# Performance work log

Measured on AMD Instinct MI355X. Metric: run time of the kernel, lower is better.

Reference implementation:

```python
import jax, jax.numpy as jnp
import numpy as np

N = 50000      # nodes
E = 800000     # edges (before self loops)
DIN = 128      # input feature dim
H = 2          # attention heads
C = 64         # per-head hidden channels (hidden_dim)
HC = H * C     # 128, concat output width of each GATv2 layer
DOUT = 4       # NUM_LANES
NEG = 0.2      # GATv2 default negative_slope


def _w(key, fan_in, shape):
    return jax.random.normal(key, shape, dtype=jnp.float32) * (1.0 / np.sqrt(fan_in))


def setup_inputs() -> dict:
    key = jax.random.key(0)
    ks = jax.random.split(key, 32)
    inp = {
        "x": jax.random.normal(ks[0], (N, DIN), dtype=jnp.float32),
        "edge_index": jax.random.randint(ks[1], (2, E), 0, N, dtype=jnp.int64),
    }
    # layer 1: DIN -> H*C
    inp["W1l"] = _w(ks[2], DIN, (DIN, HC)); inp["b1l"] = jnp.zeros((HC,), jnp.float32)
    inp["W1r"] = _w(ks[3], DIN, (DIN, HC)); inp["b1r"] = jnp.zeros((HC,), jnp.float32)
    inp["att1"] = _w(ks[4], C, (H, C));     inp["bias1"] = jnp.zeros((HC,), jnp.float32)
    # layer 2: H*C -> H*C
    inp["W2l"] = _w(ks[5], HC, (HC, HC));   inp["b2l"] = jnp.zeros((HC,), jnp.float32)
    inp["W2r"] = _w(ks[6], HC, (HC, HC));   inp["b2r"] = jnp.zeros((HC,), jnp.float32)
    inp["att2"] = _w(ks[7], C, (H, C));     inp["bias2"] = jnp.zeros((HC,), jnp.float32)
    # layer 3: H*C -> H*C
    inp["W3l"] = _w(ks[8], HC, (HC, HC));   inp["b3l"] = jnp.zeros((HC,), jnp.float32)
    inp["W3r"] = _w(ks[9], HC, (HC, HC));   inp["b3r"] = jnp.zeros((HC,), jnp.float32)
    inp["att3"] = _w(ks[10], C, (H, C));    inp["bias3"] = jnp.zeros((HC,), jnp.float32)
    # output linear
    inp["Wout"] = _w(ks[11], HC, (HC, DOUT)); inp["bout"] = jnp.zeros((DOUT,), jnp.float32)
    return inp


def gat_layer(x, src, dst, Wl, bl, Wr, br, att, bias):
    # GATv2Conv, concat=True, add_self_loops already in src/dst.
    n = x.shape[0]
    h, c = att.shape
    xl = (x @ Wl + bl).reshape(n, h, c)   # source transform
    xr = (x @ Wr + br).reshape(n, h, c)   # target transform
    m = xl[src] + xr[dst]                               # [Etot, H, C]
    e = jnp.sum(jax.nn.leaky_relu(m, NEG) * att, -1)    # [Etot, H]
    emax = jax.ops.segment_max(e, dst, num_segments=n)  # segment softmax over in-edges
    p = jnp.exp(e - emax[dst])
    denom = jax.ops.segment_sum(p, dst, num_segments=n)
    alpha = p / denom[dst]                              # [Etot, H]
    out = jax.ops.segment_sum(alpha[:, :, None] * xl[src], dst, num_segments=n)
    return out.reshape(n, h * c) + bias


def reference(x, edge_index, W1l, b1l, W1r, b1r, att1, bias1,
              W2l, b2l, W2r, b2r, att2, bias2,
              W3l, b3l, W3r, b3r, att3, bias3, Wout, bout):
    n = x.shape[0]
    loop = jnp.arange(n, dtype=edge_index.dtype)
    src = jnp.concatenate([edge_index[0], loop])  # add self loops (PyG default)
    dst = jnp.concatenate([edge_index[1], loop])
    h = jax.nn.relu(gat_layer(x, src, dst, W1l, b1l, W1r, b1r, att1, bias1))
    h = jax.nn.relu(gat_layer(h, src, dst, W2l, b2l, W2r, b2r, att2, bias2))
    h = jax.nn.relu(gat_layer(h, src, dst, W3l, b3l, W3r, b3r, att3, bias3))
    return h @ Wout + bout
```

## Files before the change

kernel.cpp:

```cpp
#include <hip/hip_runtime.h>
#include <math.h>

#define DIN  128
#define HC   128
#define NEG  0.2f

typedef __attribute__((ext_vector_type(8))) short bf16x8;
typedef __attribute__((ext_vector_type(4))) float f32x4;
typedef __attribute__((ext_vector_type(8))) _Float16 half8;
typedef __attribute__((ext_vector_type(2))) _Float16 half2v;

__device__ __forceinline__ unsigned short f2bf_rne(float x) {
    unsigned u = __float_as_uint(x);
    unsigned r = u + 0x7FFFu + ((u >> 16) & 1u);
    return (unsigned short)(r >> 16);
}
__device__ __forceinline__ float bf2f(unsigned short h) {
    return __uint_as_float(((unsigned)h) << 16);
}

__device__ __forceinline__ int colOf(int p) {
    return ((p >> 5) * 2 + (p & 1)) * 16 + ((p & 31) >> 1);
}

template <int CTRL>
__device__ __forceinline__ float dpp_xadd(float x) {
    int r = __builtin_amdgcn_update_dpp(0, __float_as_int(x), CTRL, 0xF, 0xF, true);
    return x + __int_as_float(r);
}
__device__ __forceinline__ float rowsum8(float x) {
    x = dpp_xadd<0xB1>(x);
    x = dpp_xadd<0x4E>(x);
    x = dpp_xadd<0x141>(x);
    return x;
}
__device__ __forceinline__ float rowsum16(float x) {
    x = dpp_xadd<0xB1>(x);
    x = dpp_xadd<0x4E>(x);
    x = dpp_xadd<0x141>(x);
    x = dpp_xadd<0x140>(x);
    return x;
}

__global__ void hist_kernel(const int* __restrict__ ei, int E, int N,
                            int* __restrict__ counts) {
    int i = blockIdx.x * blockDim.x + threadIdx.x;
    int Etot = E + N;
    if (i >= Etot) return;
    int dst = (i < E) ? ei[E + i] : (i - E);
    if (dst < 0 || dst >= N) return;
    atomicAdd(&counts[dst], 1);
}

__global__ void scan_kernel(const int* __restrict__ counts,
                            int* __restrict__ rowptr,
                            int* __restrict__ cursor, int n) {
    __shared__ int wsum[16];
    int tid  = threadIdx.x;
    int lane = tid & 63, wid = tid >> 6;
    int running = 0;
    for (int base = 0; base < n; base += 4096) {
        int i = base + tid * 4;
        int4 v = make_int4(0, 0, 0, 0);
        if (i < n) v = *(const int4*)&counts[i];
        int ssum = v.x + v.y + v.z + v.w;
        int x = ssum;
        #pragma unroll
        for (int off = 1; off < 64; off <<= 1) {
            int y = __shfl_up(x, off, 64);
            if (lane >= off) x += y;
        }
        if (lane == 63) wsum[wid] = x;
        __syncthreads();
        if (tid < 16) {
            int w = wsum[tid];
            #pragma unroll
            for (int off = 1; off < 16; off <<= 1) {
                int y = __shfl_up(w, off, 64);
                if (tid >= off) w += y;
            }
            wsum[tid] = w;
        }
        __syncthreads();
        int excl = running + (wid ? wsum[wid - 1] : 0) + (x - ssum);
        if (i < n) {
            int4 r;
            r.x = excl;
            r.y = r.x + v.x;
            r.z = r.y + v.y;
            r.w = r.z + v.z;
            *(int4*)&rowptr[i] = r;
            *(int4*)&cursor[i] = r;
        }
        running += wsum[15];
        __syncthreads();
    }
    if (tid == 0) rowptr[n] = running;
}

__global__ void scatter_kernel(const int* __restrict__ ei, int E, int N,
                               int* __restrict__ cursor,
                               int* __restrict__ esrc) {
    int i = blockIdx.x * blockDim.x + threadIdx.x;
    int Etot = E + N;
    if (i >= Etot) return;
    int src = (i < E) ? ei[i]     : (i - E);
    int dst = (i < E) ? ei[E + i] : (i - E);
    if (dst < 0 || dst >= N || src < 0 || src >= N) return;
    int pos = atomicAdd(&cursor[dst], 1);
    esrc[pos] = src;
}

__global__ __launch_bounds__(256) void prep_w(
        const float* __restrict__ W1l, const float* __restrict__ W1r,
        const float* __restrict__ W2l, const float* __restrict__ W2r,
        const float* __restrict__ W3l, const float* __restrict__ W3r,
        unsigned short* __restrict__ hi, unsigned short* __restrict__ lo) {
    int m = blockIdx.y;
    const float* W = (m == 0) ? W1l : (m == 1) ? W1r : (m == 2) ? W2l
                   : (m == 3) ? W2r : (m == 4) ? W3l : W3r;
    int t = blockIdx.x * 256 + threadIdx.x;
    int kb = t >> 9, nf = (t >> 6) & 7, l = t & 63;
    int col = nf * 16 + (l & 15);
    int k0  = kb * 32 + (l >> 4) * 8;
    size_t ob = ((size_t)m * 2048 + t) * 8;
    #pragma unroll
    for (int j = 0; j < 8; ++j) {
        int k = k0 + j;
        int krow = (m >= 2) ? colOf(k) : k;
        float v = W[(size_t)krow * 128 + col];
        unsigned short h = f2bf_rne(v);
        hi[ob + j] = h;
        lo[ob + j] = f2bf_rne(v - bf2f(h));
    }
}

__global__ __launch_bounds__(256) void gemm_mfma_dual(
        const float* __restrict__ X,
        const unsigned short* __restrict__ Whi,
        const unsigned short* __restrict__ Wlo, int matbase,
        const float* __restrict__ bl, const float* __restrict__ br,
        _Float16* __restrict__ xlh, _Float16* __restrict__ xrh, int nrows) {
    const unsigned short* hpl = Whi + ((size_t)(matbase + 0) * 16384);
    const unsigned short* lpl = Wlo + ((size_t)(matbase + 0) * 16384);
    const unsigned short* hpr = Whi + ((size_t)(matbase + 1) * 16384);
    const unsigned short* lpr = Wlo + ((size_t)(matbase + 1) * 16384);

    int tid = threadIdx.x;
    int w   = tid >> 6;
    int l   = tid & 63;
    int m15 = l & 15, g = l >> 4;
    int rowbase = blockIdx.x * 64 + w * 16;

    f32x4 accl[8], accr[8];
    #pragma unroll
    for (int nf = 0; nf < 8; ++nf) {
        accl[nf] = (f32x4){0.f, 0.f, 0.f, 0.f};
        accr[nf] = (f32x4){0.f, 0.f, 0.f, 0.f};
    }

    #pragma unroll
    for (int kb = 0; kb < 4; ++kb) {
        int arow = rowbase + m15;
        float4 x0 = make_float4(0.f, 0.f, 0.f, 0.f), x1 = x0;
        if (arow < nrows) {
            const float* xp = &X[(size_t)arow * 128 + kb * 32 + g * 8];
            x0 = *(const float4*)xp;
            x1 = *(const float4*)(xp + 4);
        }
        float xv[8] = {x0.x, x0.y, x0.z, x0.w, x1.x, x1.y, x1.z, x1.w};
        bf16x8 ahi, alo;
        #pragma unroll
        for (int j = 0; j < 8; ++j) {
            unsigned short h = f2bf_rne(xv[j]);
            ahi[j] = (short)h;
            alo[j] = (short)f2bf_rne(xv[j] - bf2f(h));
        }
        #pragma unroll
        for (int nf = 0; nf < 8; ++nf) {
            size_t off = (((size_t)kb * 8 + nf) * 64 + l) * 8;
            bf16x8 bhl = *(const bf16x8*)&hpl[off];
            bf16x8 bll = *(const bf16x8*)&lpl[off];
            bf16x8 bhr = *(const bf16x8*)&hpr[off];
            bf16x8 blr = *(const bf16x8*)&lpr[off];
            accl[nf] = __builtin_amdgcn_mfma_f32_16x16x32_bf16(ahi, bhl, accl[nf], 0, 0, 0);
            accl[nf] = __builtin_amdgcn_mfma_f32_16x16x32_bf16(ahi, bll, accl[nf], 0, 0, 0);
            accl[nf] = __builtin_amdgcn_mfma_f32_16x16x32_bf16(alo, bhl, accl[nf], 0, 0, 0);
            accr[nf] = __builtin_amdgcn_mfma_f32_16x16x32_bf16(ahi, bhr, accr[nf], 0, 0, 0);
            accr[nf] = __builtin_amdgcn_mfma_f32_16x16x32_bf16(ahi, blr, accr[nf], 0, 0, 0);
            accr[nf] = __builtin_amdgcn_mfma_f32_16x16x32_bf16(alo, bhr, accr[nf], 0, 0, 0);
        }
    }

    float vbl[8], vbr[8];
    #pragma unroll
    for (int nf = 0; nf < 8; ++nf) {
        vbl[nf] = bl[nf * 16 + m15];
        vbr[nf] = br[nf * 16 + m15];
    }

    #pragma unroll
    for (int a = 0; a < 4; ++a) {
        #pragma unroll
        for (int r = 0; r < 4; ++r) {
            int row = rowbase + g * 4 + r;
            if (row >= nrows) continue;
            size_t off = (size_t)row * 128 + a * 32 + m15 * 2;
            half2v pl, pr;
            pl[0] = (_Float16)(accl[2 * a][r]     + vbl[2 * a]);
            pl[1] = (_Float16)(accl[2 * a + 1][r] + vbl[2 * a + 1]);
            pr[0] = (_Float16)(accr[2 * a][r]     + vbr[2 * a]);
            pr[1] = (_Float16)(accr[2 * a + 1][r] + vbr[2 * a + 1]);
            *(half2v*)&xlh[off] = pl;
            *(half2v*)&xrh[off] = pr;
        }
    }
}

__global__ __launch_bounds__(256) void gat_aggregate(
        const _Float16* __restrict__ xlh, const _Float16* __restrict__ xrh,
        const int* __restrict__ rowptr, const int* __restrict__ esrc,
        const float* __restrict__ att, const float* __restrict__ bias,
        float* __restrict__ hout, int n, int do_relu,
        const float* __restrict__ Wout, const float* __restrict__ bout,
        float* __restrict__ out4) {
    int node = (int)((blockIdx.x * blockDim.x + threadIdx.x) >> 6);
    int lane = threadIdx.x & 63;
    if (node >= n) return;
    int g    = lane >> 4;
    int gl   = lane & 15;
    int pos0 = gl * 8;

    half8 xr8 = *(const half8*)&xrh[(size_t)node * 128 + pos0];
    float xrf[8], atp[8], atn[8];
    #pragma unroll
    for (int i = 0; i < 8; ++i) {
        float a = att[colOf(pos0 + i)];
        atp[i] = a;
        atn[i] = NEG * a;
        xrf[i] = (float)xr8[i];
    }

    float s = 0.f;
    float acc[8];
    #pragma unroll
    for (int i = 0; i < 8; ++i) acc[i] = 0.f;

    int pbeg = rowptr[node], pend = rowptr[node + 1];
    int p = pbeg + g;
    bool v0 = p < pend;
    bool v1 = p + 4 < pend;
    half8 r0 = (half8)(_Float16)0.f, r1 = r0;
    if (v0) r0 = *(const half8*)&xlh[(size_t)esrc[p] * 128 + pos0];
    if (v1) r1 = *(const half8*)&xlh[(size_t)esrc[p + 4] * 128 + pos0];

    while (v0) {
        bool v2 = p + 8 < pend;
        half8 r2 = (half8)(_Float16)0.f;
        if (v2) r2 = *(const half8*)&xlh[(size_t)esrc[p + 8] * 128 + pos0];

        float av[8], t = 0.f;
        #pragma unroll
        for (int i = 0; i < 8; ++i) {
            av[i] = (float)r0[i];
            float v = av[i] + xrf[i];
            t += v * (v > 0.f ? atp[i] : atn[i]);
        }
        t = rowsum8(t);
        float pp = __expf(fminf(t, 80.f));
        s += pp;
        #pragma unroll
        for (int i = 0; i < 8; ++i) acc[i] += pp * av[i];

        r0 = r1; r1 = r2; v0 = v1; v1 = v2; p += 4;
    }

    #pragma unroll
    for (int off = 16; off <= 32; off <<= 1) {
        s += __shfl_xor(s, off, 64);
        #pragma unroll
        for (int i = 0; i < 8; ++i) acc[i] += __shfl_xor(acc[i], off, 64);
    }

    float inv = 1.f / s;

    if (out4) {
        float o[8];
        #pragma unroll
        for (int i = 0; i < 8; ++i) {
            o[i] = acc[i] * inv + bias[colOf(pos0 + i)];
            if (do_relu) o[i] = fmaxf(o[i], 0.f);
        }
        float p0 = 0.f, p1 = 0.f, p2 = 0.f, p3 = 0.f;
        #pragma unroll
        for (int i = 0; i < 8; ++i) {
            float4 wv = *(const float4*)&Wout[colOf(pos0 + i) * 4];
            p0 += o[i] * wv.x; p1 += o[i] * wv.y;
            p2 += o[i] * wv.z; p3 += o[i] * wv.w;
        }
        p0 = rowsum16(p0); p1 = rowsum16(p1);
        p2 = rowsum16(p2); p3 = rowsum16(p3);
        if (lane == 0) {
            float4 ov = make_float4(p0 + bout[0], p1 + bout[1],
                                    p2 + bout[2], p3 + bout[3]);
            *(float4*)&out4[(size_t)node * 4] = ov;
        }
        return;
    }

    if (g == 0) {
        float o[8];
        #pragma unroll
        for (int i = 0; i < 8; ++i) {
            o[i] = acc[i] * inv + bias[colOf(pos0 + i)];
            if (do_relu) o[i] = fmaxf(o[i], 0.f);
        }
        float4 o0 = make_float4(o[0], o[1], o[2], o[3]);
        float4 o1 = make_float4(o[4], o[5], o[6], o[7]);
        *(float4*)&hout[(size_t)node * 128 + pos0]     = o0;
        *(float4*)&hout[(size_t)node * 128 + pos0 + 4] = o1;
    }
}

extern "C" void kernel_launch(void* const* d_in, const int* in_sizes, int n_in,
                              void* d_out, int out_size, void* d_ws,
                              size_t ws_size, hipStream_t stream) {
    const float* x    = (const float*)d_in[0];
    const int*   ei   = (const int*)  d_in[1];
    const float* W1l  = (const float*)d_in[2];
    const float* b1l  = (const float*)d_in[3];
    const float* W1r  = (const float*)d_in[4];
    const float* b1r  = (const float*)d_in[5];
    const float* att1 = (const float*)d_in[6];
    const float* bias1= (const float*)d_in[7];
    const float* W2l  = (const float*)d_in[8];
    const float* b2l  = (const float*)d_in[9];
    const float* W2r  = (const float*)d_in[10];
    const float* b2r  = (const float*)d_in[11];
    const float* att2 = (const float*)d_in[12];
    const float* bias2= (const float*)d_in[13];
    const float* W3l  = (const float*)d_in[14];
    const float* b3l  = (const float*)d_in[15];
    const float* W3r  = (const float*)d_in[16];
    const float* b3r  = (const float*)d_in[17];
    const float* att3 = (const float*)d_in[18];
    const float* bias3= (const float*)d_in[19];
    const float* Wout = (const float*)d_in[20];
    const float* bout = (const float*)d_in[21];

    int N    = in_sizes[0] / DIN;
    int E    = in_sizes[1] / 2;
    int Etot = E + N;

    char* base = (char*)d_ws;
    float* h = (float*)base;              base += (size_t)N * HC * 4;
    _Float16* xlh = (_Float16*)base;      base += (size_t)N * HC * 2;
    _Float16* xrh = (_Float16*)base;      base += (size_t)N * HC * 2;
    unsigned short* whi = (unsigned short*)base;  base += 6 * 16384 * 2;
    unsigned short* wlo = (unsigned short*)base;  base += 6 * 16384 * 2;
    int* esrc   = (int*)base;             base += (size_t)Etot * 4;
    int* rowptr = (int*)base;             base += (size_t)(((N + 1) + 3) & ~3) * 4;
    int* cursor = (int*)base;             base += (size_t)N * 4;
    int* counts = (int*)base;

    hipMemsetAsync(counts, 0, (size_t)N * sizeof(int), stream);
    hist_kernel<<<(Etot + 255) / 256, 256, 0, stream>>>(ei, E, N, counts);
    scan_kernel<<<1, 1024, 0, stream>>>(counts, rowptr, cursor, N);
    scatter_kernel<<<(Etot + 255) / 256, 256, 0, stream>>>(ei, E, N, cursor, esrc);
    prep_w<<<dim3(8, 6), 256, 0, stream>>>(W1l, W1r, W2l, W2r, W3l, W3r, whi, wlo);

    int gemm_grid = (N + 63) / 64;
    int agg_grid  = (N + 3) / 4;

    gemm_mfma_dual<<<gemm_grid, 256, 0, stream>>>(x, whi, wlo, 0, b1l, b1r, xlh, xrh, N);
    gat_aggregate<<<agg_grid, 256, 0, stream>>>(xlh, xrh, rowptr, esrc, att1, bias1,
                                                h, N, 1, nullptr, nullptr, nullptr);
    gemm_mfma_dual<<<gemm_grid, 256, 0, stream>>>(h, whi, wlo, 2, b2l, b2r, xlh, xrh, N);
    gat_aggregate<<<agg_grid, 256, 0, stream>>>(xlh, xrh, rowptr, esrc, att2, bias2,
                                                h, N, 1, nullptr, nullptr, nullptr);
    gemm_mfma_dual<<<gemm_grid, 256, 0, stream>>>(h, whi, wlo, 4, b3l, b3r, xlh, xrh, N);
    gat_aggregate<<<agg_grid, 256, 0, stream>>>(xlh, xrh, rowptr, esrc, att3, bias3,
                                                nullptr, N, 1, Wout, bout,
                                                (float*)d_out);
}
```

Before: 361.5 us.

## Switch GEMMs to single-pass fp16 MFMA and store hidden activations in fp16

Replaces the three-pass bf16 hi/lo split GEMM with a single fp16 MFMA pass using fp16-converted weights. Hidden activations between layers are stored as fp16 instead of fp32, which halves the write traffic in the aggregate kernel and the read traffic in the next GEMM. The GEMM tiling changes so that each block covers 32 rows and each wave handles half of the output columns. The cost is lower GEMM precision (fp16 inputs, about 11 bits of mantissa), with a risk of overflow or accuracy drift.

```diff
diff --git a/kernel.cpp b/kernel.cpp
--- a/kernel.cpp
+++ b/kernel.cpp
@@ -5,19 +5,9 @@
 #define HC   128
 #define NEG  0.2f
 
-typedef __attribute__((ext_vector_type(8))) short bf16x8;
 typedef __attribute__((ext_vector_type(4))) float f32x4;
 typedef __attribute__((ext_vector_type(8))) _Float16 half8;
 typedef __attribute__((ext_vector_type(2))) _Float16 half2v;
-
-__device__ __forceinline__ unsigned short f2bf_rne(float x) {
-    unsigned u = __float_as_uint(x);
-    unsigned r = u + 0x7FFFu + ((u >> 16) & 1u);
-    return (unsigned short)(r >> 16);
-}
-__device__ __forceinline__ float bf2f(unsigned short h) {
-    return __uint_as_float(((unsigned)h) << 16);
-}
 
 __device__ __forceinline__ int colOf(int p) {
     return ((p >> 5) * 2 + (p & 1)) * 16 + ((p & 31) >> 1);
@@ -111,11 +101,11 @@
     esrc[pos] = src;
 }
 
-__global__ __launch_bounds__(256) void prep_w(
+__global__ __launch_bounds__(256) void prep_w16(
         const float* __restrict__ W1l, const float* __restrict__ W1r,
         const float* __restrict__ W2l, const float* __restrict__ W2r,
         const float* __restrict__ W3l, const float* __restrict__ W3r,
-        unsigned short* __restrict__ hi, unsigned short* __restrict__ lo) {
+        _Float16* __restrict__ w16) {
     int m = blockIdx.y;
     const float* W = (m == 0) ? W1l : (m == 1) ? W1r : (m == 2) ? W2l
                    : (m == 3) ? W2r : (m == 4) ? W3l : W3r;
@@ -128,100 +118,96 @@
     for (int j = 0; j < 8; ++j) {
         int k = k0 + j;
         int krow = (m >= 2) ? colOf(k) : k;
-        float v = W[(size_t)krow * 128 + col];
-        unsigned short h = f2bf_rne(v);
-        hi[ob + j] = h;
-        lo[ob + j] = f2bf_rne(v - bf2f(h));
-    }
-}
-
-__global__ __launch_bounds__(256) void gemm_mfma_dual(
-        const float* __restrict__ X,
-        const unsigned short* __restrict__ Whi,
-        const unsigned short* __restrict__ Wlo, int matbase,
-        const float* __restrict__ bl, const float* __restrict__ br,
+        w16[ob + j] = (_Float16)W[(size_t)krow * 128 + col];
+    }
+}
+
+#define GEMM_BODY(A_LOAD)                                                     \
+    const _Float16* hpl = W16 + ((size_t)(matbase + 0) * 16384);              \
+    const _Float16* hpr = W16 + ((size_t)(matbase + 1) * 16384);              \
+    int tid = threadIdx.x;                                                    \
+    int w   = tid >> 6;                                                       \
+    int l   = tid & 63;                                                       \
+    int m15 = l & 15, g = l >> 4;                                             \
+    int rowbase = blockIdx.x * 32 + (w >> 1) * 16;                            \
+    int nfb     = (w & 1) * 4;                                                \
+    f32x4 accl[4], accr[4];                                                   \
+    _Pragma("unroll")                                                         \
+    for (int i = 0; i < 4; ++i) {                                             \
+        accl[i] = (f32x4){0.f, 0.f, 0.f, 0.f};                                \
+        accr[i] = (f32x4){0.f, 0.f, 0.f, 0.f};                                \
+    }                                                                         \
+    _Pragma("unroll")                                                         \
+    for (int kb = 0; kb < 4; ++kb) {                                          \
+        int arow = rowbase + m15;                                             \
+        half8 a16 = (half8)(_Float16)0.f;                                     \
+        A_LOAD                                                                \
+        _Pragma("unroll")                                                     \
+        for (int nfi = 0; nfi < 4; ++nfi) {                                   \
+            int nf = nfb + nfi;                                               \
+            size_t off = (((size_t)kb * 8 + nf) * 64 + l) * 8;                \
+            half8 b_l = *(const half8*)&hpl[off];                             \
+            half8 b_r = *(const half8*)&hpr[off];                             \
+            accl[nfi] = __builtin_amdgcn_mfma_f32_16x16x32_f16(a16, b_l, accl[nfi], 0, 0, 0); \
+            accr[nfi] = __builtin_amdgcn_mfma_f32_16x16x32_f16(a16, b_r, accr[nfi], 0, 0, 0); \
+        }                                                                     \
+    }                                                                         \
+    float vbl[4], vbr[4];                                                     \
+    _Pragma("unroll")                                                         \
+    for (int nfi = 0; nfi < 4; ++nfi) {                                       \
+        vbl[nfi] = bl[(nfb + nfi) * 16 + m15];                                \
+        vbr[nfi] = br[(nfb + nfi) * 16 + m15];                                \
+    }                                                                         \
+    _Pragma("unroll")                                                         \
+    for (int a2 = 0; a2 < 2; ++a2) {                                          \
+        int a = (nfb >> 1) + a2;                                              \
+        _Pragma("unroll")                                                     \
+        for (int r = 0; r < 4; ++r) {                                         \
+            int row = rowbase + g * 4 + r;                                    \
+            if (row >= nrows) continue;                                       \
+            size_t off = (size_t)row * 128 + a * 32 + m15 * 2;                \
+            half2v pl, pr;                                                    \
+            pl[0] = (_Float16)(accl[2 * a2][r]     + vbl[2 * a2]);            \
+            pl[1] = (_Float16)(accl[2 * a2 + 1][r] + vbl[2 * a2 + 1]);        \
+            pr[0] = (_Float16)(accr[2 * a2][r]     + vbr[2 * a2]);            \
+            pr[1] = (_Float16)(accr[2 * a2 + 1][r] + vbr[2 * a2 + 1]);        \
+            *(half2v*)&xlh[off] = pl;                                         \
+            *(half2v*)&xrh[off] = pr;                                         \
+        }                                                                     \
+    }
+
+__global__ __launch_bounds__(256) void gemm_f16_from_f32(
+        const float* __restrict__ X, const _Float16* __restrict__ W16,
+        int matbase, const float* __restrict__ bl, const float* __restrict__ br,
         _Float16* __restrict__ xlh, _Float16* __restrict__ xrh, int nrows) {
-    const unsigned short* hpl = Whi + ((size_t)(matbase + 0) * 16384);
-    const unsigned short* lpl = Wlo + ((size_t)(matbase + 0) * 16384);
-    const unsigned short* hpr = Whi + ((size_t)(matbase + 1) * 16384);
-    const unsigned short* lpr = Wlo + ((size_t)(matbase + 1) * 16384);
-
-    int tid = threadIdx.x;
-    int w   = tid >> 6;
-    int l   = tid & 63;
-    int m15 = l & 15, g = l >> 4;
-    int rowbase = blockIdx.x * 64 + w * 16;
-
-    f32x4 accl[8], accr[8];
-    #pragma unroll
-    for (int nf = 0; nf < 8; ++nf) {
-        accl[nf] = (f32x4){0.f, 0.f, 0.f, 0.f};
-        accr[nf] = (f32x4){0.f, 0.f, 0.f, 0.f};
-    }
-
-    #pragma unroll
-    for (int kb = 0; kb < 4; ++kb) {
-        int arow = rowbase + m15;
-        float4 x0 = make_float4(0.f, 0.f, 0.f, 0.f), x1 = x0;
+    GEMM_BODY(
         if (arow < nrows) {
             const float* xp = &X[(size_t)arow * 128 + kb * 32 + g * 8];
-            x0 = *(const float4*)xp;
-            x1 = *(const float4*)(xp + 4);
-        }
-        float xv[8] = {x0.x, x0.y, x0.z, x0.w, x1.x, x1.y, x1.z, x1.w};
-        bf16x8 ahi, alo;
-        #pragma unroll
-        for (int j = 0; j < 8; ++j) {
-            unsigned short h = f2bf_rne(xv[j]);
-            ahi[j] = (short)h;
-            alo[j] = (short)f2bf_rne(xv[j] - bf2f(h));
-        }
-        #pragma unroll
-        for (int nf = 0; nf < 8; ++nf) {
-            size_t off = (((size_t)kb * 8 + nf) * 64 + l) * 8;
-            bf16x8 bhl = *(const bf16x8*)&hpl[off];
-            bf16x8 bll = *(const bf16x8*)&lpl[off];
-            bf16x8 bhr = *(const bf16x8*)&hpr[off];
-            bf16x8 blr = *(const bf16x8*)&lpr[off];
-            accl[nf] = __builtin_amdgcn_mfma_f32_16x16x32_bf16(ahi, bhl, accl[nf], 0, 0, 0);
-            accl[nf] = __builtin_amdgcn_mfma_f32_16x16x32_bf16(ahi, bll, accl[nf], 0, 0, 0);
-            accl[nf] = __builtin_amdgcn_mfma_f32_16x16x32_bf16(alo, bhl, accl[nf], 0, 0, 0);
-            accr[nf] = __builtin_amdgcn_mfma_f32_16x16x32_bf16(ahi, bhr, accr[nf], 0, 0, 0);
-            accr[nf] = __builtin_amdgcn_mfma_f32_16x16x32_bf16(ahi, blr, accr[nf], 0, 0, 0);
-            accr[nf] = __builtin_amdgcn_mfma_f32_16x16x32_bf16(alo, bhr, accr[nf], 0, 0, 0);
-        }
-    }
-
-    float vbl[8], vbr[8];
-    #pragma unroll
-    for (int nf = 0; nf < 8; ++nf) {
-        vbl[nf] = bl[nf * 16 + m15];
-        vbr[nf] = br[nf * 16 + m15];
-    }
-
-    #pragma unroll
-    for (int a = 0; a < 4; ++a) {
-        #pragma unroll
-        for (int r = 0; r < 4; ++r) {
-            int row = rowbase + g * 4 + r;
-            if (row >= nrows) continue;
-            size_t off = (size_t)row * 128 + a * 32 + m15 * 2;
-            half2v pl, pr;
-            pl[0] = (_Float16)(accl[2 * a][r]     + vbl[2 * a]);
-            pl[1] = (_Float16)(accl[2 * a + 1][r] + vbl[2 * a + 1]);
-            pr[0] = (_Float16)(accr[2 * a][r]     + vbr[2 * a]);
-            pr[1] = (_Float16)(accr[2 * a + 1][r] + vbr[2 * a + 1]);
-            *(half2v*)&xlh[off] = pl;
-            *(half2v*)&xrh[off] = pr;
-        }
-    }
+            float4 x0 = *(const float4*)xp;
+            float4 x1 = *(const float4*)(xp + 4);
+            a16[0] = (_Float16)x0.x; a16[1] = (_Float16)x0.y;
+            a16[2] = (_Float16)x0.z; a16[3] = (_Float16)x0.w;
+            a16[4] = (_Float16)x1.x; a16[5] = (_Float16)x1.y;
+            a16[6] = (_Float16)x1.z; a16[7] = (_Float16)x1.w;
+        }
+    )
+}
+
+__global__ __launch_bounds__(256) void gemm_f16_from_f16(
+        const _Float16* __restrict__ X, const _Float16* __restrict__ W16,
+        int matbase, const float* __restrict__ bl, const float* __restrict__ br,
+        _Float16* __restrict__ xlh, _Float16* __restrict__ xrh, int nrows) {
+    GEMM_BODY(
+        if (arow < nrows)
+            a16 = *(const half8*)&X[(size_t)arow * 128 + kb * 32 + g * 8];
+    )
 }
 
 __global__ __launch_bounds__(256) void gat_aggregate(
         const _Float16* __restrict__ xlh, const _Float16* __restrict__ xrh,
         const int* __restrict__ rowptr, const int* __restrict__ esrc,
         const float* __restrict__ att, const float* __restrict__ bias,
-        float* __restrict__ hout, int n, int do_relu,
+        _Float16* __restrict__ hout, int n, int do_relu,
         const float* __restrict__ Wout, const float* __restrict__ bout,
         float* __restrict__ out4) {
     int node = (int)((blockIdx.x * blockDim.x + threadIdx.x) >> 6);
@@ -309,16 +295,14 @@
     }
 
     if (g == 0) {
-        float o[8];
+        half8 oh;
         #pragma unroll
         for (int i = 0; i < 8; ++i) {
-            o[i] = acc[i] * inv + bias[colOf(pos0 + i)];
-            if (do_relu) o[i] = fmaxf(o[i], 0.f);
-        }
-        float4 o0 = make_float4(o[0], o[1], o[2], o[3]);
-        float4 o1 = make_float4(o[4], o[5], o[6], o[7]);
-        *(float4*)&hout[(size_t)node * 128 + pos0]     = o0;
-        *(float4*)&hout[(size_t)node * 128 + pos0 + 4] = o1;
+            float o = acc[i] * inv + bias[colOf(pos0 + i)];
+            if (do_relu) o = fmaxf(o, 0.f);
+            oh[i] = (_Float16)o;
+        }
+        *(half8*)&hout[(size_t)node * 128 + pos0] = oh;
     }
 }
 
@@ -353,11 +337,10 @@
     int Etot = E + N;
 
     char* base = (char*)d_ws;
-    float* h = (float*)base;              base += (size_t)N * HC * 4;
+    _Float16* h16 = (_Float16*)base;      base += (size_t)N * HC * 2;
     _Float16* xlh = (_Float16*)base;      base += (size_t)N * HC * 2;
     _Float16* xrh = (_Float16*)base;      base += (size_t)N * HC * 2;
-    unsigned short* whi = (unsigned short*)base;  base += 6 * 16384 * 2;
-    unsigned short* wlo = (unsigned short*)base;  base += 6 * 16384 * 2;
+    _Float16* w16 = (_Float16*)base;      base += 6 * 16384 * 2;
     int* esrc   = (int*)base;             base += (size_t)Etot * 4;
     int* rowptr = (int*)base;             base += (size_t)(((N + 1) + 3) & ~3) * 4;
     int* cursor = (int*)base;             base += (size_t)N * 4;
@@ -367,18 +350,18 @@
     hist_kernel<<<(Etot + 255) / 256, 256, 0, stream>>>(ei, E, N, counts);
     scan_kernel<<<1, 1024, 0, stream>>>(counts, rowptr, cursor, N);
     scatter_kernel<<<(Etot + 255) / 256, 256, 0, stream>>>(ei, E, N, cursor, esrc);
-    prep_w<<<dim3(8, 6), 256, 0, stream>>>(W1l, W1r, W2l, W2r, W3l, W3r, whi, wlo);
-
-    int gemm_grid = (N + 63) / 64;
+    prep_w16<<<dim3(8, 6), 256, 0, stream>>>(W1l, W1r, W2l, W2r, W3l, W3r, w16);
+
+    int gemm_grid = (N + 31) / 32;
     int agg_grid  = (N + 3) / 4;
 
-    gemm_mfma_dual<<<gemm_grid, 256, 0, stream>>>(x, whi, wlo, 0, b1l, b1r, xlh, xrh, N);
+    gemm_f16_from_f32<<<gemm_grid, 256, 0, stream>>>(x, w16, 0, b1l, b1r, xlh, xrh, N);
     gat_aggregate<<<agg_grid, 256, 0, stream>>>(xlh, xrh, rowptr, esrc, att1, bias1,
-                                                h, N, 1, nullptr, nullptr, nullptr);
-    gemm_mfma_dual<<<gemm_grid, 256, 0, stream>>>(h, whi, wlo, 2, b2l, b2r, xlh, xrh, N);
+                                                h16, N, 1, nullptr, nullptr, nullptr);
+    gemm_f16_from_f16<<<gemm_grid, 256, 0, stream>>>(h16, w16, 2, b2l, b2r, xlh, xrh, N);
     gat_aggregate<<<agg_grid, 256, 0, stream>>>(xlh, xrh, rowptr, esrc, att2, bias2,
-                                                h, N, 1, nullptr, nullptr, nullptr);
-    gemm_mfma_dual<<<gemm_grid, 256, 0, stream>>>(h, whi, wlo, 4, b3l, b3r, xlh, xrh, N);
+                                                h16, N, 1, nullptr, nullptr, nullptr);
+    gemm_f16_from_f16<<<gemm_grid, 256, 0, stream>>>(h16, w16, 4, b3l, b3r, xlh, xrh, N);
     gat_aggregate<<<agg_grid, 256, 0, stream>>>(xlh, xrh, rowptr, esrc, att3, bias3,
                                                 nullptr, N, 1, Wout, bout,
                                                 (float*)d_out);
```

Result: faster. 320.4 us (-11.3%).
